# Kernel tuning notes

Hardware: AMD Instinct MI355X
Metric: run time of the kernel (lower is better)

Reference implementation:

```python
import jax, jax.numpy as jnp
from jax import lax
import numpy as np

B, L, C, PRED = 64, 512, 321, 96
PATCH, STRIDE = 16, 8
N = (L - PATCH) // STRIDE + 1 + 1  # 64 patches (after replication pad)
HID = PATCH * 2                    # expansion_factor=2
ALPHA, EPS = 0.2, 1e-5

def gelu(v):
    return jax.nn.gelu(v, approximate=False)  # torch nn.GELU default (erf)

def setup_inputs() -> dict:
    key = jax.random.key(0)
    ks = jax.random.split(key, 10)
    init = lambda k, s: (jax.random.normal(k, s) * 0.02).astype(jnp.float32)
    return dict(
        x=jax.random.normal(ks[0], (B, L, C), jnp.float32),
        rev_w=jnp.ones((C,), jnp.float32), rev_b=jnp.zeros((C,), jnp.float32),
        fc1_w=init(ks[1], (HID, PATCH)), fc1_b=jnp.zeros((HID,), jnp.float32),
        bn1_w=jnp.ones((N,), jnp.float32), bn1_b=jnp.zeros((N,), jnp.float32),
        conv_w=init(ks[2], (N, 1, 3)), conv_b=jnp.zeros((N,), jnp.float32),
        bn2_w=jnp.ones((N,), jnp.float32), bn2_b=jnp.zeros((N,), jnp.float32),
        fc2_w=init(ks[3], (PATCH, HID)), fc2_b=jnp.zeros((PATCH,), jnp.float32),
        m1_w=init(ks[4], (2 * N, N)), m1_b=jnp.zeros((2 * N,), jnp.float32),
        m2_w=init(ks[5], (N, 2 * N)), m2_b=jnp.zeros((N,), jnp.float32),
        gl_scale=jnp.full((1,), 0.1, jnp.float32),
        ln_w=jnp.ones((PATCH,), jnp.float32), ln_b=jnp.zeros((PATCH,), jnp.float32),
        seas_w=init(ks[6], (PRED, N * PATCH)), seas_b=jnp.zeros((PRED,), jnp.float32),
        tr_w=init(ks[7], (PRED, L)), tr_b=jnp.zeros((PRED,), jnp.float32),
        fus_w=init(ks[8], (PRED, 2 * PRED)), fus_b=jnp.zeros((PRED,), jnp.float32),
    )

def _batchnorm(h, w, b):
    # BatchNorm1d over channel axis N (train-mode batch stats, biased var)
    mu = h.mean((0, 2), keepdims=True)
    var = h.var((0, 2), keepdims=True)
    return (h - mu) * lax.rsqrt(var + EPS) * w[None, :, None] + b[None, :, None]

def reference(x, rev_w, rev_b, fc1_w, fc1_b, bn1_w, bn1_b, conv_w, conv_b,
              bn2_w, bn2_b, fc2_w, fc2_b, m1_w, m1_b, m2_w, m2_b, gl_scale,
              ln_w, ln_b, seas_w, seas_b, tr_w, tr_b, fus_w, fus_b):
    # --- RevIN norm (torch std is unbiased, ddof=1) ---
    mean = x.mean(1, keepdims=True)
    std = jnp.std(x, axis=1, ddof=1, keepdims=True) + EPS
    xn = (x - mean) / std * rev_w + rev_b
    # --- EMA trend/seasonal decomposition via scan ---
    xt = jnp.moveaxis(xn, 1, 0)                      # [L,B,C]
    def step(c, xi):
        t = ALPHA * xi + (1.0 - ALPHA) * c
        return t, t
    _, rest = lax.scan(step, xt[0], xt[1:])
    trend = jnp.moveaxis(jnp.concatenate([xt[:1], rest], 0), 0, 1)  # [B,L,C]
    seasonal = xn - trend
    # --- patching (replication pad right by STRIDE, unfold) ---
    s = seasonal.transpose(0, 2, 1).reshape(B * C, L)
    s = jnp.concatenate([s, jnp.broadcast_to(s[:, -1:], (B * C, STRIDE))], axis=1)
    idx = np.arange(N)[:, None] * STRIDE + np.arange(PATCH)[None, :]
    sp = s[:, idx]                                    # [B*C, N, PATCH]
    # --- IntraPatch (local): fc1 -> GELU -> BN -> depthwise conv -> GELU -> BN -> fc2 + res ---
    h = gelu(sp @ fc1_w.T + fc1_b)                    # [BC,N,HID]
    h = _batchnorm(h, bn1_w, bn1_b)
    h = lax.conv_general_dilated(h, conv_w, (1,), ((1, 1),),
                                 feature_group_count=N,
                                 dimension_numbers=('NCH', 'OIH', 'NCH'))
    h = h + conv_b[None, :, None]
    h = _batchnorm(gelu(h), bn2_w, bn2_b)
    local = h @ fc2_w.T + fc2_b + sp                  # dropout is identity (eval)
    # --- InterPatch (global): pool -> MLP -> sigmoid gate ---
    pooled = sp.mean(-1)                              # [BC,N]
    w = jax.nn.sigmoid(gelu(pooled @ m1_w.T + m1_b) @ m2_w.T + m2_b)
    glob = sp * (1.0 + gl_scale * w[..., None])
    # --- fusion 'add' + residual LayerNorm over PATCH ---
    y = sp + local + glob
    mu = y.mean(-1, keepdims=True)
    var = y.var(-1, keepdims=True)
    y = (y - mu) * lax.rsqrt(var + EPS) * ln_w + ln_b
    # --- heads ---
    s_pred = y.reshape(B * C, N * PATCH) @ seas_w.T + seas_b
    t = trend.transpose(0, 2, 1).reshape(B * C, L)
    t_pred = t @ tr_w.T + tr_b
    out = jnp.concatenate([s_pred, t_pred], -1) @ fus_w.T + fus_b
    out = out.reshape(B, C, PRED).transpose(0, 2, 1)  # [B,PRED,C]
    # --- RevIN denorm ---
    out = (out - rev_b) / rev_w
    return out * std + mean
```

## Files before the change

### kernel.cpp

```cpp
#include <hip/hip_runtime.h>
#include <hip/hip_bf16.h>
#include <hip/hip_fp16.h>
#include <math.h>

#define B_    64
#define L_    512
#define C_    321
#define PRED_ 96
#define N_    64
#define HID_  32
#define BC_   (B_*C_)
#define SROW_ 528
#define EPS_  1e-5f
#define ALPHA_ 0.2f
#define GR_   16
#define RB_   8
#define NBLK2_ (BC_/GR_)
#define NBLKH_ (BC_/8)
#define D64_  6.2771017353866808e-7f
#define STW_  548
#define UTW_  260

typedef __attribute__((ext_vector_type(8))) short bf16x8;
typedef __attribute__((ext_vector_type(4))) float f32x4;

__device__ __forceinline__ float gelu_f(float x){
  float ax = fabsf(x);
  float z  = ax * 0.70710678118654752440f;
  float t  = __builtin_amdgcn_rcpf(fmaf(0.3275911f, z, 1.0f));
  float poly = fmaf(fmaf(fmaf(fmaf(1.061405429f, t, -1.453152027f),
                   t, 1.421413741f), t, -0.284496736f), t, 0.254829592f) * t;
  float e  = __expf(-z*z);
  float erfp = fmaf(-poly, e, 1.0f);
  return fmaf(0.5f*ax, erfp, 0.5f*x);
}
__device__ __forceinline__ unsigned short bf16bits(float x){
  __hip_bfloat16 h = __float2bfloat16(x);
  return *(unsigned short*)&h;
}
__device__ __forceinline__ unsigned short f16bits(float x){
  __half h = __float2half(x);
  return *(unsigned short*)&h;
}
__device__ __forceinline__ float f16val(unsigned short u){
  __half h = *(__half*)&u;
  return __half2float(h);
}
__device__ __forceinline__ bf16x8 cvt8(const float* p){
  float4 a = *(const float4*)p;
  float4 b = *(const float4*)(p+4);
  bf16x8 v;
  v[0]=(short)bf16bits(a.x); v[1]=(short)bf16bits(a.y);
  v[2]=(short)bf16bits(a.z); v[3]=(short)bf16bits(a.w);
  v[4]=(short)bf16bits(b.x); v[5]=(short)bf16bits(b.y);
  v[6]=(short)bf16bits(b.z); v[7]=(short)bf16bits(b.w);
  return v;
}

__global__ __launch_bounds__(256) void k1_all(
    const float* __restrict__ x, const float* __restrict__ rev_w, const float* __restrict__ rev_b,
    const float* __restrict__ seas_w, const float* __restrict__ tr_w, const float* __restrict__ fus_w,
    const float* __restrict__ seas_b, const float* __restrict__ tr_b, const float* __restrict__ fus_b,
    const float* __restrict__ fc2_w,
    float* __restrict__ s_raw, __hip_bfloat16* __restrict__ t_bf, float* __restrict__ rowpar,
    float* __restrict__ pooled,
    __hip_bfloat16* __restrict__ Wsf, __hip_bfloat16* __restrict__ Wtf,
    float* __restrict__ biasc, float* __restrict__ colsumT, float* __restrict__ Wsum) {
  __shared__ float lf[8][32];
  __shared__ float psum[8][32], psq[8][32];
  __shared__ float fs[8][32];
  __shared__ float st[32*STW_];
  int tid = threadIdx.x;
  int bid = blockIdx.x;
  if (bid >= BC_/32) {
    int fb = bid - BC_/32;
    if (fb < 576) {
      int idx = fb*256 + tid;
      int j = idx / 1536, k = idx - j*1536;
      float acc = 0.f;
      if (k < 1024) {
        for (int i=0;i<96;++i) acc = fmaf(fus_w[j*192+i], seas_w[i*1024+k], acc);
        Wsf[(size_t)j*1024 + k] = __float2bfloat16(acc);
      } else {
        int l = k - 1024;
        for (int i=0;i<96;++i) acc = fmaf(fus_w[j*192+96+i], tr_w[i*512+l], acc);
        Wtf[(size_t)j*512 + l] = __float2bfloat16(acc);
      }
    } else {
      __shared__ float rowsum[96];
      if (tid >= 96 && tid < 112) {
        int j = tid - 96;
        float s = 0.f;
        #pragma unroll
        for (int k=0;k<32;++k) s += fc2_w[j*32+k];
        Wsum[j] = s;
      }
      if (tid < 96) {
        float s = 0.f;
        for (int l=0;l<512;++l) s += tr_w[tid*512+l];
        rowsum[tid] = s;
      }
      __syncthreads();
      if (tid < 96) {
        float acc = fus_b[tid], cs = 0.f;
        for (int i=0;i<96;++i) {
          acc = fmaf(fus_w[tid*192+i],    seas_b[i], acc);
          acc = fmaf(fus_w[tid*192+96+i], tr_b[i],   acc);
          cs  = fmaf(fus_w[tid*192+96+i], rowsum[i], cs);
        }
        biasc[tid] = acc; colsumT[tid] = cs;
      }
    }
    return;
  }
  int q = tid >> 5, r = tid & 31;
  int row0 = bid*32;
  int row = row0 + r;
  int b = row / C_, c = row - b*C_;
  const float* xp = x + (size_t)b*L_*C_ + c;
  int l0 = q*64;
  float sreg[64];
  float loc = 0.f, sum = 0.f, sq = 0.f;
  #pragma unroll
  for (int i=0;i<64;++i) {
    float v = xp[(size_t)(l0+i)*C_];
    sum += v; sq = fmaf(v,v,sq);
    loc = (q==0 && i==0) ? v : fmaf(ALPHA_, v, 0.8f*loc);
    sreg[i] = loc;
  }
  lf[q][r] = loc; psum[q][r] = sum; psq[q][r] = sq;
  __syncthreads();
  float cin = 0.f;
  for (int j=0;j<q;++j) cin = fmaf(D64_, cin, lf[j][r]);
  float S=0.f, Q=0.f;
  #pragma unroll
  for (int qq=0;qq<8;++qq){ S += psum[qq][r]; Q += psq[qq][r]; }
  float mean = S*(1.0f/512.0f);
  float var  = (Q - S*S*(1.0f/512.0f))*(1.0f/511.0f);
  var = fmaxf(var, 0.f);
  float stdv = sqrtf(var) + EPS_;
  float rwc = rev_w[c];
  float a = rwc / stdv;
  if (q==0) {
    float rbc = rev_b[c];
    float g = rbc - mean*a;
    float inva = stdv / rwc;
    ((float4*)rowpar)[row] = make_float4(a, g, mean, inva);
  }
  float prev = 0.f, f = 1.f, slast = 0.f;
  float sums8[8];
  #pragma unroll
  for (int j=0;j<8;++j) sums8[j] = 0.f;
  #pragma unroll
  for (int i=0;i<64;++i) {
    float lc = sreg[i];
    f *= 0.8f;
    float s = (q==0 && i==0) ? 0.f : fmaf(4.f, lc - prev, -f*cin);
    prev = lc;
    float sv = s * a;
    st[r*STW_ + q*64 + i] = sv;
    sums8[i>>3] += sv;
    slast = sv;
  }
  fs[q][r] = sums8[0];
  if (q==7) {
    #pragma unroll
    for (int k=0;k<8;++k) st[r*STW_ + 512 + k] = slast;
  }
  __syncthreads();
  for (int idx=tid; idx<32*130; idx+=256) {
    int rr = idx/130, g = idx - rr*130;
    float4 v = *(float4*)&st[rr*STW_ + g*4];
    *(float4*)&s_raw[(size_t)(row0+rr)*SROW_ + g*4] = v;
  }
  {
    float nf = (q < 7) ? fs[q+1][r] : 8.0f*slast;
    #pragma unroll
    for (int j=0;j<7;++j)
      pooled[(size_t)row*64 + q*8 + j] = (sums8[j] + sums8[j+1])*(1.0f/16.0f);
    pooled[(size_t)row*64 + q*8 + 7] = (sums8[7] + nf)*(1.0f/16.0f);
  }
  __syncthreads();
  unsigned* tb = (unsigned*)st;
  {
    float f2 = 1.f; unsigned lo = 0;
    #pragma unroll
    for (int i=0;i<64;++i) {
      f2 *= 0.8f;
      float tt = fmaf(f2, cin, sreg[i]) * a;
      unsigned hb = bf16bits(tt);
      if ((i&1)==0) lo = hb;
      else tb[r*UTW_ + q*32 + (i>>1)] = lo | (hb<<16);
    }
  }
  __syncthreads();
  for (int idx=tid; idx<32*64; idx+=256) {
    int rr = idx>>6, g = idx&63;
    uint4 v = *(uint4*)&tb[rr*UTW_ + g*4];
    *(uint4*)&t_bf[(size_t)(row0+rr)*512 + g*8] = v;
  }
}

__global__ __launch_bounds__(512) void k4_gate(
    const float* __restrict__ pooled,
    const float* __restrict__ m1_w, const float* __restrict__ m1_b,
    const float* __restrict__ m2_w, const float* __restrict__ m2_b,
    float* __restrict__ wl_g) {
  __shared__ __align__(16) __hip_bfloat16 buf[17408];
  int t = threadIdx.x;
  int row0 = blockIdx.x*64;
  __hip_bfloat16* A1 = buf;
  __hip_bfloat16* B1 = buf + 4608;
  __hip_bfloat16* H1 = buf;
  __hip_bfloat16* B2 = buf + 8704;
  for (int idx=t; idx<4096; idx+=512) {
    int r = idx>>6, k = idx&63;
    A1[r*72+k] = __float2bfloat16(pooled[(size_t)(row0+r)*64 + k]);
  }
  for (int idx=t; idx<8192; idx+=512) {
    int r = idx>>6, k = idx&63;
    B1[r*72+k] = __float2bfloat16(m1_w[idx]);
  }
  __syncthreads();
  int lane = t & 63, w = t >> 6;
  int fr = lane & 15, fg = lane >> 4;
  int mt = w & 3;
  int ng0 = (w>>2)*4;
  f32x4 acc1[4];
  #pragma unroll
  for (int nn=0;nn<4;++nn) acc1[nn] = (f32x4){0.f,0.f,0.f,0.f};
  #pragma unroll
  for (int ksub=0; ksub<2; ++ksub) {
    bf16x8 av = *(bf16x8*)&A1[(mt*16+fr)*72 + ksub*32 + fg*8];
    #pragma unroll
    for (int nn=0;nn<4;++nn) {
      bf16x8 bv = *(bf16x8*)&B1[((ng0+nn)*16+fr)*72 + ksub*32 + fg*8];
      acc1[nn] = __builtin_amdgcn_mfma_f32_16x16x32_bf16(av, bv, acc1[nn], 0,0,0);
    }
  }
  __syncthreads();
  #pragma unroll
  for (int nn=0;nn<4;++nn) {
    int col = (ng0+nn)*16 + fr;
    float bias = m1_b[col];
    #pragma unroll
    for (int reg=0;reg<4;++reg) {
      int row = mt*16 + fg*4 + reg;
      H1[row*136 + col] = __float2bfloat16(gelu_f(acc1[nn][reg] + bias));
    }
  }
  for (int idx=t; idx<8192; idx+=512) {
    int r = idx>>7, k = idx&127;
    B2[r*136+k] = __float2bfloat16(m2_w[idx]);
  }
  __syncthreads();
  int nt0 = (w>>2)*2;
  f32x4 acc2[2];
  #pragma unroll
  for (int nn=0;nn<2;++nn) acc2[nn] = (f32x4){0.f,0.f,0.f,0.f};
  #pragma unroll
  for (int ksub=0; ksub<4; ++ksub) {
    bf16x8 av = *(bf16x8*)&H1[(mt*16+fr)*136 + ksub*32 + fg*8];
    #pragma unroll
    for (int nn=0;nn<2;++nn) {
      bf16x8 bv = *(bf16x8*)&B2[((nt0+nn)*16+fr)*136 + ksub*32 + fg*8];
      acc2[nn] = __builtin_amdgcn_mfma_f32_16x16x32_bf16(av, bv, acc2[nn], 0,0,0);
    }
  }
  #pragma unroll
  for (int nn=0;nn<2;++nn) {
    int col = (nt0+nn)*16 + fr;
    float bias = m2_b[col];
    #pragma unroll
    for (int reg=0;reg<4;++reg) {
      int row = mt*16 + fg*4 + reg;
      wl_g[(size_t)(row0+row)*64 + col] = 1.0f/(1.0f + __expf(-(acc2[nn][reg] + bias)));
    }
  }
}

__global__ __launch_bounds__(256) void k2_bn1stats(
    const float* __restrict__ s_raw,
    const float* __restrict__ fc1_w, const float* __restrict__ fc1_b,
    float* __restrict__ partials) {
  __shared__ float sl[GR_*SROW_];
  __shared__ float red[2][GR_*64];
  int t = threadIdx.x;
  int row0 = blockIdx.x*GR_;
  for (int idx=t; idx<GR_*520; idx+=256) {
    int rr = idx/520, cc = idx - rr*520;
    sl[rr*SROW_+cc] = s_raw[(size_t)(row0+rr)*SROW_+cc];
  }
  __syncthreads();
  int lr = t >> 4, ng = t & 15;
  for (int q=0;q<4;++q) {
    int n = ng + 16*q;
    float sp[16];
    #pragma unroll
    for (int p=0;p<16;++p) sp[p] = sl[lr*SROW_ + n*8 + p];
    float s1=0.f, s2=0.f;
    #pragma unroll
    for (int hid=0; hid<32; ++hid) {
      float acc = fc1_b[hid];
      #pragma unroll
      for (int p=0;p<16;++p) acc = fmaf(sp[p], fc1_w[hid*16+p], acc);
      float gv = gelu_f(acc);
      s1 += gv; s2 = fmaf(gv,gv,s2);
    }
    red[0][lr*64+n] = s1;
    red[1][lr*64+n] = s2;
  }
  __syncthreads();
  if (t < 64) {
    float S1=0.f, S2=0.f;
    for (int lr2=0; lr2<GR_; ++lr2) { S1 += red[0][lr2*64+t]; S2 += red[1][lr2*64+t]; }
    partials[((size_t)blockIdx.x*64+t)*2+0] = S1;
    partials[((size_t)blockIdx.x*64+t)*2+1] = S2;
  }
}

__global__ __launch_bounds__(512) void k2v5_bn1_cr(
    const float* __restrict__ s_raw,
    const float* __restrict__ fc1_w, const float* __restrict__ fc1_b,
    const float* __restrict__ conv_w,
    float* __restrict__ partials, __hip_bfloat16* __restrict__ crp) {
  __shared__ __align__(16) __hip_bfloat16 Hb[4*512*8];
  __shared__ float cw[192];
  __shared__ float red[2][512];
  int t = threadIdx.x;
  int row0 = blockIdx.x*8;
  if (t < 192) cw[t] = conv_w[t];
  int lane = t & 63, w = t >> 6;
  int fr = lane & 15, fg = lane >> 4;
  bf16x8 z8 = (bf16x8){0,0,0,0,0,0,0,0};
  bf16x8 wv0 = (fg < 2) ? cvt8(&fc1_w[(0*16+fr)*16 + fg*8]) : z8;
  bf16x8 wv1 = (fg < 2) ? cvt8(&fc1_w[(1*16+fr)*16 + fg*8]) : z8;
  f32x4 acc[4][2];
  #pragma unroll
  for (int mt=0;mt<4;++mt)
    #pragma unroll
    for (int nt=0;nt<2;++nt) acc[mt][nt] = (f32x4){0.f,0.f,0.f,0.f};
  #pragma unroll
  for (int mt=0;mt<4;++mt) {
    int p = (w*4+mt)*16 + fr;
    int lr = p>>6, n = p&63;
    bf16x8 pv = (fg < 2) ? cvt8(&s_raw[(size_t)(row0+lr)*SROW_ + n*8 + fg*8]) : z8;
    acc[mt][0] = __builtin_amdgcn_mfma_f32_16x16x32_bf16(wv0, pv, acc[mt][0], 0,0,0);
    acc[mt][1] = __builtin_amdgcn_mfma_f32_16x16x32_bf16(wv1, pv, acc[mt][1], 0,0,0);
  }
  #pragma unroll
  for (int mt=0;mt<4;++mt) {
    int p = (w*4+mt)*16 + fr;
    #pragma unroll
    for (int nt=0;nt<2;++nt) {
      float4 b4 = ((const float4*)fc1_b)[nt*4+fg];
      float g0 = gelu_f(acc[mt][nt][0] + b4.x);
      float g1 = gelu_f(acc[mt][nt][1] + b4.y);
      float g2 = gelu_f(acc[mt][nt][2] + b4.z);
      float g3 = gelu_f(acc[mt][nt][3] + b4.w);
      unsigned lo = (unsigned)bf16bits(g0) | (((unsigned)bf16bits(g1))<<16);
      unsigned hi = (unsigned)bf16bits(g2) | (((unsigned)bf16bits(g3))<<16);
      int hb = nt*16 + fg*4;
      *(uint2*)&Hb[(hb>>3)*4096 + p*8 + (hb&7)] = make_uint2(lo, hi);
    }
  }
  __syncthreads();
  {
    int n = t & 63;
    uint4 u0 = *(const uint4*)&Hb[0*4096 + t*8];
    uint4 u1 = *(const uint4*)&Hb[1*4096 + t*8];
    uint4 u2 = *(const uint4*)&Hb[2*4096 + t*8];
    uint4 u3 = *(const uint4*)&Hb[3*4096 + t*8];
    unsigned uw[16] = {u0.x,u0.y,u0.z,u0.w, u1.x,u1.y,u1.z,u1.w,
                       u2.x,u2.y,u2.z,u2.w, u3.x,u3.y,u3.z,u3.w};
    float g[32];
    #pragma unroll
    for (int j=0;j<16;++j) {
      g[2*j]   = __uint_as_float(uw[j]<<16);
      g[2*j+1] = __uint_as_float(uw[j] & 0xffff0000u);
    }
    float s1=0.f, s2=0.f;
    #pragma unroll
    for (int k=0;k<32;++k) { s1 += g[k]; s2 = fmaf(g[k], g[k], s2); }
    float w0=cw[n*3], wm=cw[n*3+1], wp=cw[n*3+2];
    unsigned wds[16]; unsigned crlo = 0;
    float prevv = 0.f;
    #pragma unroll
    for (int k=0;k<32;++k) {
      float cr = fmaf(prevv, w0, fmaf(g[k], wm, (k<31) ? g[k+1]*wp : 0.f));
      prevv = g[k];
      unsigned hbits = bf16bits(cr);
      if ((k&1)==0) crlo = hbits; else wds[k>>1] = crlo | (hbits<<16);
    }
    uint4* dst = (uint4*)&crp[((size_t)row0*64 + t)*32];
    dst[0] = make_uint4(wds[0],wds[1],wds[2],wds[3]);
    dst[1] = make_uint4(wds[4],wds[5],wds[6],wds[7]);
    dst[2] = make_uint4(wds[8],wds[9],wds[10],wds[11]);
    dst[3] = make_uint4(wds[12],wds[13],wds[14],wds[15]);
    red[0][t] = s1;
    red[1][t] = s2;
  }
  __syncthreads();
  if (t < 64) {
    float S1=0.f, S2=0.f;
    #pragma unroll
    for (int lr2=0; lr2<8; ++lr2) { S1 += red[0][lr2*64+t]; S2 += red[1][lr2*64+t]; }
    partials[((size_t)blockIdx.x*64+t)*2+0] = S1;
    partials[((size_t)blockIdx.x*64+t)*2+1] = S2;
  }
}

__global__ __launch_bounds__(256) void k_bnreduce(
    const float* __restrict__ partials, int nblk,
    const float* __restrict__ bnw, const float* __restrict__ bnb,
    float* __restrict__ scale, float* __restrict__ shift) {
  __shared__ float red[2][256];
  int n = blockIdx.x, t = threadIdx.x;
  float s1=0.f, s2=0.f;
  for (int i=t; i<nblk; i+=256) {
    s1 += partials[((size_t)i*64+n)*2+0];
    s2 += partials[((size_t)i*64+n)*2+1];
  }
  red[0][t]=s1; red[1][t]=s2;
  __syncthreads();
  for (int off=128; off>0; off>>=1) {
    if (t<off) { red[0][t]+=red[0][t+off]; red[1][t]+=red[1][t+off]; }
    __syncthreads();
  }
  if (t==0) {
    const float count = (float)BC_ * 32.0f;
    float mu = red[0][0]/count;
    float var = red[1][0]/count - mu*mu;
    float sc = rsqrtf(var + EPS_) * bnw[n];
    scale[n] = sc;
    shift[n] = bnb[n] - mu*sc;
  }
}

__global__ __launch_bounds__(256) void k3_bn2stats(
    const float* __restrict__ s_raw,
    const float* __restrict__ fc1_w, const float* __restrict__ fc1_b,
    const float* __restrict__ scale1, const float* __restrict__ shift1,
    const float* __restrict__ conv_w, const float* __restrict__ conv_b,
    float* __restrict__ partials) {
  __shared__ float sl[GR_*SROW_];
  __shared__ float sc1[64], sh1[64], cw[192], cb[64];
  __shared__ float red[2][GR_*64];
  int t = threadIdx.x;
  int row0 = blockIdx.x*GR_;
  if (t < 64) { sc1[t]=scale1[t]; sh1[t]=shift1[t]; cb[t]=conv_b[t]; }
  if (t >= 64 && t < 256) cw[t-64] = conv_w[t-64];
  __syncthreads();
  for (int idx=t; idx<GR_*520; idx+=256) {
    int rr = idx/520, cc = idx - rr*520;
    sl[rr*SROW_+cc] = s_raw[(size_t)(row0+rr)*SROW_+cc];
  }
  __syncthreads();
  int lr = t >> 4, ng = t & 15;
  for (int q=0;q<4;++q) {
    int n = ng + 16*q;
    float sp[16];
    #pragma unroll
    for (int p=0;p<16;++p) sp[p] = sl[lr*SROW_ + n*8 + p];
    float scn = sc1[n], shn = sh1[n];
    float h[32];
    #pragma unroll
    for (int hid=0; hid<32; ++hid) {
      float acc = fc1_b[hid];
      #pragma unroll
      for (int p=0;p<16;++p) acc = fmaf(sp[p], fc1_w[hid*16+p], acc);
      h[hid] = fmaf(gelu_f(acc), scn, shn);
    }
    float w0=cw[n*3], wm=cw[n*3+1], wpp=cw[n*3+2], cbn=cb[n];
    float s1=0.f, s2=0.f, prev=0.f;
    #pragma unroll
    for (int k2=0;k2<32;++k2) {
      float cur = h[k2];
      float cv = cbn;
      cv = fmaf(prev, w0, cv);
      cv = fmaf(cur, wm, cv);
      if (k2<31) cv = fmaf(h[k2+1], wpp, cv);
      float gv = gelu_f(cv);
      s1 += gv; s2 = fmaf(gv,gv,s2);
      prev = cur;
    }
    red[0][lr*64+n]=s1; red[1][lr*64+n]=s2;
  }
  __syncthreads();
  if (t < 64) {
    float S1=0.f, S2=0.f;
    for (int lr2=0; lr2<GR_; ++lr2) { S1 += red[0][lr2*64+t]; S2 += red[1][lr2*64+t]; }
    partials[((size_t)blockIdx.x*64+t)*2+0] = S1;
    partials[((size_t)blockIdx.x*64+t)*2+1] = S2;
  }
}

__global__ __launch_bounds__(512) void k3v3_bn2_u(
    const __hip_bfloat16* __restrict__ crp,
    const float* __restrict__ scale1, const float* __restrict__ shift1,
    const float* __restrict__ conv_w, const float* __restrict__ conv_b,
    const float* __restrict__ fc2_w,
    float* __restrict__ partials, __half* __restrict__ Ub) {
  __shared__ float sc1[64], sh0l[64], shml[64], sh31l[64];
  __shared__ float red[2][512];
  int t = threadIdx.x;
  int row0 = blockIdx.x*8;
  if (t < 64) {
    float w0=conv_w[t*3], wm=conv_w[t*3+1], wp=conv_w[t*3+2];
    float s1v=shift1[t], cbv=conv_b[t];
    sc1[t]  = scale1[t];
    sh0l[t] = fmaf(s1v, wm+wp, cbv);
    shml[t] = fmaf(s1v, w0+wm+wp, cbv);
    sh31l[t]= fmaf(s1v, w0+wm, cbv);
  }
  __syncthreads();
  int n = t&63;
  const uint4* crb = (const uint4*)&crp[((size_t)row0*64 + t)*32];
  uint4 u0=crb[0], u1=crb[1], u2=crb[2], u3=crb[3];
  unsigned uw[16] = {u0.x,u0.y,u0.z,u0.w, u1.x,u1.y,u1.z,u1.w,
                     u2.x,u2.y,u2.z,u2.w, u3.x,u3.y,u3.z,u3.w};
  float sc1n = sc1[n];
  float shm = shml[n];
  float g[32];
  float s1=0.f, s2=0.f;
  #pragma unroll
  for (int j=0;j<16;++j) {
    unsigned u = uw[j];
    float c0 = __uint_as_float(u<<16);
    float c1 = __uint_as_float(u & 0xffff0000u);
    float sh_0 = (j==0)  ? sh0l[n]  : shm;
    float sh_1 = (j==15) ? sh31l[n] : shm;
    float g0 = gelu_f(fmaf(c0, sc1n, sh_0));
    float g1 = gelu_f(fmaf(c1, sc1n, sh_1));
    g[2*j]   = g0;
    g[2*j+1] = g1;
    s1 += g0 + g1;
    s2 = fmaf(g0,g0, fmaf(g1,g1, s2));
  }
  unsigned wds[8];
  #pragma unroll
  for (int jj=0;jj<8;++jj) {
    float ua = 0.f, ub = 0.f;
    #pragma unroll
    for (int k=0;k<32;++k) {
      ua = fmaf(fc2_w[(2*jj  )*32+k], g[k], ua);
      ub = fmaf(fc2_w[(2*jj+1)*32+k], g[k], ub);
    }
    wds[jj] = (unsigned)f16bits(ua) | (((unsigned)f16bits(ub))<<16);
  }
  uint4* dst = (uint4*)&Ub[((size_t)row0*64 + t)*16];
  dst[0] = make_uint4(wds[0],wds[1],wds[2],wds[3]);
  dst[1] = make_uint4(wds[4],wds[5],wds[6],wds[7]);
  red[0][t]=s1; red[1][t]=s2;
  __syncthreads();
  if (t < 64) {
    float S1=0.f, S2=0.f;
    #pragma unroll
    for (int lr2=0; lr2<8; ++lr2) { S1 += red[0][lr2*64+t]; S2 += red[1][lr2*64+t]; }
    partials[((size_t)blockIdx.x*64+t)*2+0] = S1;
    partials[((size_t)blockIdx.x*64+t)*2+1] = S2;
  }
}

__global__ __launch_bounds__(256) void k5a_pipeline(
    const float* __restrict__ s_raw, const float* __restrict__ wl_g,
    const float* __restrict__ fc1_w, const float* __restrict__ fc1_b,
    const float* __restrict__ scale1, const float* __restrict__ shift1,
    const float* __restrict__ conv_w, const float* __restrict__ conv_b,
    const float* __restrict__ scale2, const float* __restrict__ shift2,
    const float* __restrict__ fc2_w, const float* __restrict__ fc2_b,
    const float* __restrict__ gl_scale,
    const float* __restrict__ ln_w, const float* __restrict__ ln_b,
    __hip_bfloat16* __restrict__ ybf) {
  __shared__ float sl[RB_*SROW_];
  __shared__ float cw[192], cb[64];
  __shared__ float sc1[64], sh1[64], sc2[64], sh2[64];
  int t = threadIdx.x;
  int row0 = blockIdx.x*RB_;
  if (t<64) { sc1[t]=scale1[t]; sh1[t]=shift1[t]; sc2[t]=scale2[t]; sh2[t]=shift2[t]; cb[t]=conv_b[t]; }
  if (t>=64 && t<256) cw[t-64]=conv_w[t-64];
  __syncthreads();
  for (int idx=t; idx<RB_*520; idx+=256) {
    int rr = idx/520, cc = idx - rr*520;
    sl[rr*SROW_+cc] = s_raw[(size_t)(row0+rr)*SROW_+cc];
  }
  __syncthreads();
  float glv = gl_scale[0];
  for (int idx=t; idx<RB_*64; idx+=256) {
    int rr = idx>>6, n = idx&63;
    float wlv = wl_g[(size_t)row0*64 + idx];
    float h[32];
    {
      float sp[16];
      #pragma unroll
      for (int p=0;p<16;++p) sp[p] = sl[rr*SROW_ + n*8 + p];
      float scn=sc1[n], shn=sh1[n];
      #pragma unroll
      for (int hid=0;hid<32;++hid) {
        float acc=fc1_b[hid];
        #pragma unroll
        for (int p=0;p<16;++p) acc=fmaf(sp[p], fc1_w[hid*16+p], acc);
        h[hid]=fmaf(gelu_f(acc), scn, shn);
      }
    }
    {
      float w0=cw[n*3], wm=cw[n*3+1], wpp=cw[n*3+2], cbn=cb[n];
      float sc2n=sc2[n], sh2n=sh2[n];
      float prev=0.f;
      #pragma unroll
      for (int k2=0;k2<32;++k2) {
        float cur = h[k2];
        float cv = cbn;
        cv = fmaf(prev, w0, cv);
        cv = fmaf(cur, wm, cv);
        if (k2<31) cv = fmaf(h[k2+1], wpp, cv);
        h[k2] = fmaf(gelu_f(cv), sc2n, sh2n);
        prev = cur;
      }
    }
    float yv[16];
    #pragma unroll
    for (int p=0;p<16;++p) {
      float acc=fc2_b[p];
      #pragma unroll
      for (int hid=0;hid<32;++hid) acc=fmaf(h[hid], fc2_w[p*32+hid], acc);
      yv[p]=acc;
    }
    float smul = 3.0f + glv*wlv;
    float mu=0.f;
    #pragma unroll
    for (int p=0;p<16;++p) {
      yv[p]=fmaf(sl[rr*SROW_ + n*8 + p], smul, yv[p]);
      mu+=yv[p];
    }
    mu *= (1.0f/16.0f);
    float var=0.f;
    #pragma unroll
    for (int p=0;p<16;++p){ float d=yv[p]-mu; var=fmaf(d,d,var); }
    var *= (1.0f/16.0f);
    float rs = rsqrtf(var + EPS_);
    unsigned int wds[8];
    #pragma unroll
    for (int j=0;j<8;++j) {
      unsigned int lo = bf16bits(fmaf((yv[2*j]-mu)*rs,   ln_w[2*j],   ln_b[2*j]));
      unsigned int hi = bf16bits(fmaf((yv[2*j+1]-mu)*rs, ln_w[2*j+1], ln_b[2*j+1]));
      wds[j] = lo | (hi<<16);
    }
    size_t ybase = (size_t)(row0+rr)*1024 + n*16;
    uint4* dst = (uint4*)&ybf[ybase];
    dst[0] = make_uint4(wds[0],wds[1],wds[2],wds[3]);
    dst[1] = make_uint4(wds[4],wds[5],wds[6],wds[7]);
  }
}

__global__ __launch_bounds__(512) void k5a_v4(
    const float* __restrict__ s_raw, const float* __restrict__ wl_g,
    const float* __restrict__ scale2, const float* __restrict__ shift2,
    const float* __restrict__ Wsum, const float* __restrict__ fc2_b,
    const float* __restrict__ gl_scale,
    const float* __restrict__ ln_w, const float* __restrict__ ln_b,
    __hip_bfloat16* __restrict__ ybf) {
  __shared__ float sc2l[64], sh2l[64];
  int t = threadIdx.x;
  int row0 = blockIdx.x*RB_;
  if (t < 64) { sc2l[t]=scale2[t]; sh2l[t]=shift2[t]; }
  __syncthreads();
  int rr = t>>6, n = t&63;
  int row = row0 + rr;
  float glv = gl_scale[0];
  float wlv = wl_g[(size_t)row*64 + n];
  size_t pbase = ((size_t)row*64 + n)*16;
  uint4* uptr = (uint4*)&ybf[pbase];
  uint4 a = uptr[0], b = uptr[1];
  unsigned hw[8] = {a.x,a.y,a.z,a.w, b.x,b.y,b.z,b.w};
  float sc2n = sc2l[n], sh2n = sh2l[n];
  float yv[16];
  #pragma unroll
  for (int j=0;j<8;++j) {
    float U0 = f16val((unsigned short)(hw[j] & 0xffffu));
    float U1 = f16val((unsigned short)(hw[j] >> 16));
    yv[2*j]   = fmaf(sc2n, U0, fmaf(sh2n, Wsum[2*j],   fc2_b[2*j]));
    yv[2*j+1] = fmaf(sc2n, U1, fmaf(sh2n, Wsum[2*j+1], fc2_b[2*j+1]));
  }
  const float* sp_g = &s_raw[(size_t)row*SROW_ + n*8];
  float4 s0 = *(const float4*)(sp_g);
  float4 s1v = *(const float4*)(sp_g+4);
  float4 s2v = *(const float4*)(sp_g+8);
  float4 s3 = *(const float4*)(sp_g+12);
  float sp[16] = {s0.x,s0.y,s0.z,s0.w, s1v.x,s1v.y,s1v.z,s1v.w,
                  s2v.x,s2v.y,s2v.z,s2v.w, s3.x,s3.y,s3.z,s3.w};
  float smul = 3.0f + glv*wlv;
  float mu=0.f;
  #pragma unroll
  for (int p=0;p<16;++p) {
    yv[p] = fmaf(sp[p], smul, yv[p]);
    mu += yv[p];
  }
  mu *= (1.0f/16.0f);
  float var=0.f;
  #pragma unroll
  for (int p=0;p<16;++p){ float d=yv[p]-mu; var=fmaf(d,d,var); }
  var *= (1.0f/16.0f);
  float rs = rsqrtf(var + EPS_);
  unsigned int wds[8];
  #pragma unroll
  for (int j=0;j<8;++j) {
    unsigned int lo = bf16bits(fmaf((yv[2*j]-mu)*rs,   ln_w[2*j],   ln_b[2*j]));
    unsigned int hi = bf16bits(fmaf((yv[2*j+1]-mu)*rs, ln_w[2*j+1], ln_b[2*j+1]));
    wds[j] = lo | (hi<<16);
  }
  uptr[0] = make_uint4(wds[0],wds[1],wds[2],wds[3]);
  uptr[1] = make_uint4(wds[4],wds[5],wds[6],wds[7]);
}

__global__ __launch_bounds__(384) void k5b_gemm(
    const __hip_bfloat16* __restrict__ ybf, const __hip_bfloat16* __restrict__ tbf,
    const __hip_bfloat16* __restrict__ Wsf, const __hip_bfloat16* __restrict__ Wtf,
    const float* __restrict__ rowpar, const float* __restrict__ rev_b,
    const float* __restrict__ biasc, const float* __restrict__ colsumT,
    float* __restrict__ out) {
  __shared__ __align__(16) __hip_bfloat16 As[2*16*72];
  __shared__ __align__(16) __hip_bfloat16 Bs[2*96*72];
  __shared__ float rp[64];
  __shared__ float rbl[16];
  __shared__ int   obase[16];
  __shared__ float bcl[96], csl[96];
  int tid = threadIdx.x;
  int row0 = blockIdx.x*16;
  if (tid < 64) rp[tid] = rowpar[(size_t)row0*4 + tid];
  if (tid >= 64 && tid < 80) {
    int lr = tid-64;
    int row = row0 + lr; int b = row/C_; int c = row - b*C_;
    rbl[lr] = rev_b[c]; obase[lr] = b*PRED_*C_ + c;
  }
  if (tid >= 96 && tid < 192) { bcl[tid-96]=biasc[tid-96]; csl[tid-96]=colsumT[tid-96]; }
  int lane = tid & 63, w = tid >> 6;
  int fr = lane & 15, fg = lane >> 4;
  bool a0 = tid < 128;
  int r0 = a0 ? (tid>>3) : ((tid-128)>>3);
  int c0 = a0 ? (tid&7)  : ((tid-128)&7);
  int r1 = (tid+256)>>3, c1 = (tid+256)&7;
  bool h2 = tid < 128;
  int r2 = (tid+640)>>3, c2 = (tid+640)&7;
  f32x4 acc = (f32x4){0.f,0.f,0.f,0.f};

  uint4 v0, v1, v2;
  auto LOAD = [&](int ks){
    const __hip_bfloat16* Ag; const __hip_bfloat16* Bg; int K; int kofs;
    if (ks < 8) { Ag = tbf + (size_t)row0*512;  Bg = Wtf; K = 512;  kofs = ks*64; }
    else        { Ag = ybf + (size_t)row0*1024; Bg = Wsf; K = 1024; kofs = (ks-8)*64; }
    v0 = a0 ? *(const uint4*)(Ag + (size_t)r0*K + kofs + c0*8)
            : *(const uint4*)(Bg + (size_t)r0*K + kofs + c0*8);
    v1 = *(const uint4*)(Bg + (size_t)r1*K + kofs + c1*8);
    if (h2) v2 = *(const uint4*)(Bg + (size_t)r2*K + kofs + c2*8);
  };

  LOAD(0);
  int cur = 0;
  for (int ks=0; ks<24; ++ks) {
    __hip_bfloat16* Ab = &As[cur*16*72];
    __hip_bfloat16* Bb = &Bs[cur*96*72];
    if (a0) *(uint4*)&Ab[r0*72 + c0*8] = v0;
    else    *(uint4*)&Bb[r0*72 + c0*8] = v0;
    *(uint4*)&Bb[r1*72 + c1*8] = v1;
    if (h2) *(uint4*)&Bb[r2*72 + c2*8] = v2;
    __syncthreads();
    if (ks < 23) LOAD(ks+1);
    #pragma unroll
    for (int ksub=0; ksub<2; ++ksub) {
      bf16x8 av = *(bf16x8*)&Ab[fr*72 + ksub*32 + fg*8];
      bf16x8 bv = *(bf16x8*)&Bb[(w*16+fr)*72 + ksub*32 + fg*8];
      acc = __builtin_amdgcn_mfma_f32_16x16x32_bf16(av, bv, acc, 0,0,0);
    }
    cur ^= 1;
  }
  {
    int col = w*16 + fr;
    float cs = csl[col], bc = bcl[col];
    #pragma unroll
    for (int reg=0;reg<4;++reg) {
      int rloc = fg*4 + reg;
      float g = rp[rloc*4+1], meanv = rp[rloc*4+2], inva = rp[rloc*4+3];
      float val = acc[reg] + g*cs + bc;
      val = (val - rbl[rloc])*inva + meanv;
      out[(size_t)obase[rloc] + (size_t)col*C_] = val;
    }
  }
}

extern "C" void kernel_launch(void* const* d_in, const int* in_sizes, int n_in,
                              void* d_out, int out_size, void* d_ws, size_t ws_size,
                              hipStream_t stream) {
  const float* x      = (const float*)d_in[0];
  const float* rev_w  = (const float*)d_in[1];
  const float* rev_b  = (const float*)d_in[2];
  const float* fc1_w  = (const float*)d_in[3];
  const float* fc1_b  = (const float*)d_in[4];
  const float* bn1_w  = (const float*)d_in[5];
  const float* bn1_b  = (const float*)d_in[6];
  const float* conv_w = (const float*)d_in[7];
  const float* conv_b = (const float*)d_in[8];
  const float* bn2_w  = (const float*)d_in[9];
  const float* bn2_b  = (const float*)d_in[10];
  const float* fc2_w  = (const float*)d_in[11];
  const float* fc2_b  = (const float*)d_in[12];
  const float* m1_w   = (const float*)d_in[13];
  const float* m1_b   = (const float*)d_in[14];
  const float* m2_w   = (const float*)d_in[15];
  const float* m2_b   = (const float*)d_in[16];
  const float* gl     = (const float*)d_in[17];
  const float* ln_w   = (const float*)d_in[18];
  const float* ln_b   = (const float*)d_in[19];
  const float* seas_w = (const float*)d_in[20];
  const float* seas_b = (const float*)d_in[21];
  const float* tr_w   = (const float*)d_in[22];
  const float* tr_b   = (const float*)d_in[23];
  const float* fus_w  = (const float*)d_in[24];
  const float* fus_b  = (const float*)d_in[25];
  float* out = (float*)d_out;
  float* ws = (float*)d_ws;

  __hip_bfloat16* Wsf  = (__hip_bfloat16*)(ws);
  __hip_bfloat16* Wtf  = (__hip_bfloat16*)(ws + 49152);
  float* biasc   = ws + 73728;
  float* colsumT = ws + 73856;
  float* scale1  = ws + 73984;
  float* shift1  = ws + 74048;
  float* scale2  = ws + 74112;
  float* shift2  = ws + 74176;
  float* partials= ws + 74240;
  float* Wsum    = ws + 74240;
  float* rowpar  = ws + 238592;
  float* s_raw   = ws + 320768;
  __hip_bfloat16* t_bf = (__hip_bfloat16*)(ws + 11168000);
  __hip_bfloat16* ybf  = (__hip_bfloat16*)(ws + 16427264);
  float* pooled  = ws + 26945792;
  float* wl_g    = ws + 28260608;
  __hip_bfloat16* crp  = (__hip_bfloat16*)(ws + 29575424);
  float* ppool   = ws + 26945792;
  __half* Uh     = (__half*)ybf;
  const size_t NEED = (29575424ull + 21037056ull) * 4ull;
  bool big = (ws_size >= NEED);

  hipLaunchKernelGGL(k1_all, dim3(BC_/32 + 577), dim3(256), 0, stream,
    x, rev_w, rev_b, seas_w, tr_w, fus_w, seas_b, tr_b, fus_b, fc2_w,
    s_raw, t_bf, rowpar, pooled, Wsf, Wtf, biasc, colsumT, Wsum);
  hipLaunchKernelGGL(k4_gate, dim3(BC_/64), dim3(512), 0, stream, pooled, m1_w, m1_b, m2_w, m2_b, wl_g);
  if (big) {
    hipLaunchKernelGGL(k2v5_bn1_cr, dim3(NBLKH_), dim3(512), 0, stream, s_raw, fc1_w, fc1_b, conv_w, ppool, crp);
    hipLaunchKernelGGL(k_bnreduce, dim3(64), dim3(256), 0, stream, ppool, NBLKH_, bn1_w, bn1_b, scale1, shift1);
    hipLaunchKernelGGL(k3v3_bn2_u, dim3(NBLKH_), dim3(512), 0, stream, crp, scale1, shift1, conv_w, conv_b, fc2_w, ppool, Uh);
    hipLaunchKernelGGL(k_bnreduce, dim3(64), dim3(256), 0, stream, ppool, NBLKH_, bn2_w, bn2_b, scale2, shift2);
    hipLaunchKernelGGL(k5a_v4, dim3(NBLKH_), dim3(512), 0, stream,
      s_raw, wl_g, scale2, shift2, Wsum, fc2_b, gl, ln_w, ln_b, ybf);
  } else {
    hipLaunchKernelGGL(k2_bn1stats, dim3(NBLK2_), dim3(256), 0, stream, s_raw, fc1_w, fc1_b, partials);
    hipLaunchKernelGGL(k_bnreduce, dim3(64), dim3(256), 0, stream, partials, NBLK2_, bn1_w, bn1_b, scale1, shift1);
    hipLaunchKernelGGL(k3_bn2stats, dim3(NBLK2_), dim3(256), 0, stream, s_raw, fc1_w, fc1_b, scale1, shift1, conv_w, conv_b, partials);
    hipLaunchKernelGGL(k_bnreduce, dim3(64), dim3(256), 0, stream, partials, NBLK2_, bn2_w, bn2_b, scale2, shift2);
    hipLaunchKernelGGL(k5a_pipeline, dim3(BC_/RB_), dim3(256), 0, stream,
      s_raw, wl_g, fc1_w, fc1_b, scale1, shift1, conv_w, conv_b,
      scale2, shift2, fc2_w, fc2_b, gl, ln_w, ln_b, ybf);
  }
  hipLaunchKernelGGL(k5b_gemm, dim3(BC_/16), dim3(384), 0, stream,
    ybf, t_bf, Wsf, Wtf, rowpar, rev_b, biasc, colsumT, out);
}
```

Baseline: 206.9 us.

## Recompute fc1+GELU+conv in BN2 kernel instead of storing intermediate conv tensor

The BN1 stats kernel no longer writes the bf16 conv-result intermediate (crp). It only computes the fc1 MFMA, applies GELU and reduces sums directly from registers. The BN2 kernel now rereads s_raw and recomputes fc1, GELU and the depthwise conv before applying BN1, GELU and fc2. This trades a large intermediate global write and read for duplicated MFMA and GELU compute plus an extra s_raw read, and adds register pressure from the fused loop.

```diff
diff --git a/kernel.cpp b/kernel.cpp
--- a/kernel.cpp
+++ b/kernel.cpp
@@ -319,92 +319,48 @@
   }
 }
 
-__global__ __launch_bounds__(512) void k2v5_bn1_cr(
+__global__ __launch_bounds__(512) void k2v6_bn1stats(
     const float* __restrict__ s_raw,
     const float* __restrict__ fc1_w, const float* __restrict__ fc1_b,
-    const float* __restrict__ conv_w,
-    float* __restrict__ partials, __hip_bfloat16* __restrict__ crp) {
-  __shared__ __align__(16) __hip_bfloat16 Hb[4*512*8];
-  __shared__ float cw[192];
-  __shared__ float red[2][512];
+    float* __restrict__ partials) {
+  __shared__ float red[2][4][16][33];
   int t = threadIdx.x;
   int row0 = blockIdx.x*8;
-  if (t < 192) cw[t] = conv_w[t];
   int lane = t & 63, w = t >> 6;
   int fr = lane & 15, fg = lane >> 4;
   bf16x8 z8 = (bf16x8){0,0,0,0,0,0,0,0};
-  bf16x8 wv0 = (fg < 2) ? cvt8(&fc1_w[(0*16+fr)*16 + fg*8]) : z8;
-  bf16x8 wv1 = (fg < 2) ? cvt8(&fc1_w[(1*16+fr)*16 + fg*8]) : z8;
-  f32x4 acc[4][2];
-  #pragma unroll
-  for (int mt=0;mt<4;++mt)
-    #pragma unroll
-    for (int nt=0;nt<2;++nt) acc[mt][nt] = (f32x4){0.f,0.f,0.f,0.f};
+  bf16x8 wv0 = (fg < 2) ? cvt8(&fc1_w[fr*16 + fg*8]) : z8;
+  bf16x8 wv1 = (fg < 2) ? cvt8(&fc1_w[(16+fr)*16 + fg*8]) : z8;
+  float4 b40 = ((const float4*)fc1_b)[fg];
+  float4 b41 = ((const float4*)fc1_b)[4+fg];
   #pragma unroll
   for (int mt=0;mt<4;++mt) {
     int p = (w*4+mt)*16 + fr;
     int lr = p>>6, n = p&63;
     bf16x8 pv = (fg < 2) ? cvt8(&s_raw[(size_t)(row0+lr)*SROW_ + n*8 + fg*8]) : z8;
-    acc[mt][0] = __builtin_amdgcn_mfma_f32_16x16x32_bf16(wv0, pv, acc[mt][0], 0,0,0);
-    acc[mt][1] = __builtin_amdgcn_mfma_f32_16x16x32_bf16(wv1, pv, acc[mt][1], 0,0,0);
-  }
-  #pragma unroll
-  for (int mt=0;mt<4;++mt) {
-    int p = (w*4+mt)*16 + fr;
-    #pragma unroll
-    for (int nt=0;nt<2;++nt) {
-      float4 b4 = ((const float4*)fc1_b)[nt*4+fg];
-      float g0 = gelu_f(acc[mt][nt][0] + b4.x);
-      float g1 = gelu_f(acc[mt][nt][1] + b4.y);
-      float g2 = gelu_f(acc[mt][nt][2] + b4.z);
-      float g3 = gelu_f(acc[mt][nt][3] + b4.w);
-      unsigned lo = (unsigned)bf16bits(g0) | (((unsigned)bf16bits(g1))<<16);
-      unsigned hi = (unsigned)bf16bits(g2) | (((unsigned)bf16bits(g3))<<16);
-      int hb = nt*16 + fg*4;
-      *(uint2*)&Hb[(hb>>3)*4096 + p*8 + (hb&7)] = make_uint2(lo, hi);
-    }
-  }
-  __syncthreads();
-  {
-    int n = t & 63;
-    uint4 u0 = *(const uint4*)&Hb[0*4096 + t*8];
-    uint4 u1 = *(const uint4*)&Hb[1*4096 + t*8];
-    uint4 u2 = *(const uint4*)&Hb[2*4096 + t*8];
-    uint4 u3 = *(const uint4*)&Hb[3*4096 + t*8];
-    unsigned uw[16] = {u0.x,u0.y,u0.z,u0.w, u1.x,u1.y,u1.z,u1.w,
-                       u2.x,u2.y,u2.z,u2.w, u3.x,u3.y,u3.z,u3.w};
-    float g[32];
-    #pragma unroll
-    for (int j=0;j<16;++j) {
-      g[2*j]   = __uint_as_float(uw[j]<<16);
-      g[2*j+1] = __uint_as_float(uw[j] & 0xffff0000u);
-    }
+    f32x4 a0 = (f32x4){0.f,0.f,0.f,0.f};
+    f32x4 a1 = (f32x4){0.f,0.f,0.f,0.f};
+    a0 = __builtin_amdgcn_mfma_f32_16x16x32_bf16(wv0, pv, a0, 0,0,0);
+    a1 = __builtin_amdgcn_mfma_f32_16x16x32_bf16(wv1, pv, a1, 0,0,0);
     float s1=0.f, s2=0.f;
-    #pragma unroll
-    for (int k=0;k<32;++k) { s1 += g[k]; s2 = fmaf(g[k], g[k], s2); }
-    float w0=cw[n*3], wm=cw[n*3+1], wp=cw[n*3+2];
-    unsigned wds[16]; unsigned crlo = 0;
-    float prevv = 0.f;
-    #pragma unroll
-    for (int k=0;k<32;++k) {
-      float cr = fmaf(prevv, w0, fmaf(g[k], wm, (k<31) ? g[k+1]*wp : 0.f));
-      prevv = g[k];
-      unsigned hbits = bf16bits(cr);
-      if ((k&1)==0) crlo = hbits; else wds[k>>1] = crlo | (hbits<<16);
-    }
-    uint4* dst = (uint4*)&crp[((size_t)row0*64 + t)*32];
-    dst[0] = make_uint4(wds[0],wds[1],wds[2],wds[3]);
-    dst[1] = make_uint4(wds[4],wds[5],wds[6],wds[7]);
-    dst[2] = make_uint4(wds[8],wds[9],wds[10],wds[11]);
-    dst[3] = make_uint4(wds[12],wds[13],wds[14],wds[15]);
-    red[0][t] = s1;
-    red[1][t] = s2;
+    float bb0[4] = {b40.x,b40.y,b40.z,b40.w};
+    float bb1[4] = {b41.x,b41.y,b41.z,b41.w};
+    #pragma unroll
+    for (int reg=0;reg<4;++reg) {
+      float g0 = gelu_f(a0[reg] + bb0[reg]);
+      float g1 = gelu_f(a1[reg] + bb1[reg]);
+      s1 += g0 + g1;
+      s2 = fmaf(g0,g0, fmaf(g1,g1, s2));
+    }
+    red[0][mt][fr][w*4+fg] = s1;
+    red[1][mt][fr][w*4+fg] = s2;
   }
   __syncthreads();
   if (t < 64) {
+    int mtn = t>>4, frn = t&15;
     float S1=0.f, S2=0.f;
     #pragma unroll
-    for (int lr2=0; lr2<8; ++lr2) { S1 += red[0][lr2*64+t]; S2 += red[1][lr2*64+t]; }
+    for (int i=0;i<32;++i) { S1 += red[0][mtn][frn][i]; S2 += red[1][mtn][frn][i]; }
     partials[((size_t)blockIdx.x*64+t)*2+0] = S1;
     partials[((size_t)blockIdx.x*64+t)*2+1] = S2;
   }
@@ -495,13 +451,16 @@
   }
 }
 
-__global__ __launch_bounds__(512) void k3v3_bn2_u(
-    const __hip_bfloat16* __restrict__ crp,
+__global__ __launch_bounds__(512) void k3v4_bn2_u(
+    const float* __restrict__ s_raw,
+    const float* __restrict__ fc1_w, const float* __restrict__ fc1_b,
     const float* __restrict__ scale1, const float* __restrict__ shift1,
     const float* __restrict__ conv_w, const float* __restrict__ conv_b,
     const float* __restrict__ fc2_w,
     float* __restrict__ partials, __half* __restrict__ Ub) {
+  __shared__ __align__(16) __hip_bfloat16 Hb[4*512*8];
   __shared__ float sc1[64], sh0l[64], shml[64], sh31l[64];
+  __shared__ float cw[192];
   __shared__ float red[2][512];
   int t = threadIdx.x;
   int row0 = blockIdx.x*8;
@@ -513,45 +472,82 @@
     shml[t] = fmaf(s1v, w0+wm+wp, cbv);
     sh31l[t]= fmaf(s1v, w0+wm, cbv);
   }
-  __syncthreads();
-  int n = t&63;
-  const uint4* crb = (const uint4*)&crp[((size_t)row0*64 + t)*32];
-  uint4 u0=crb[0], u1=crb[1], u2=crb[2], u3=crb[3];
-  unsigned uw[16] = {u0.x,u0.y,u0.z,u0.w, u1.x,u1.y,u1.z,u1.w,
-                     u2.x,u2.y,u2.z,u2.w, u3.x,u3.y,u3.z,u3.w};
-  float sc1n = sc1[n];
-  float shm = shml[n];
-  float g[32];
-  float s1=0.f, s2=0.f;
-  #pragma unroll
-  for (int j=0;j<16;++j) {
-    unsigned u = uw[j];
-    float c0 = __uint_as_float(u<<16);
-    float c1 = __uint_as_float(u & 0xffff0000u);
-    float sh_0 = (j==0)  ? sh0l[n]  : shm;
-    float sh_1 = (j==15) ? sh31l[n] : shm;
-    float g0 = gelu_f(fmaf(c0, sc1n, sh_0));
-    float g1 = gelu_f(fmaf(c1, sc1n, sh_1));
-    g[2*j]   = g0;
-    g[2*j+1] = g1;
-    s1 += g0 + g1;
-    s2 = fmaf(g0,g0, fmaf(g1,g1, s2));
-  }
-  unsigned wds[8];
-  #pragma unroll
-  for (int jj=0;jj<8;++jj) {
-    float ua = 0.f, ub = 0.f;
+  if (t >= 64 && t < 256) cw[t-64] = conv_w[t-64];
+  int lane = t & 63, w = t >> 6;
+  int fr = lane & 15, fg = lane >> 4;
+  bf16x8 z8 = (bf16x8){0,0,0,0,0,0,0,0};
+  bf16x8 wv0 = (fg < 2) ? cvt8(&fc1_w[fr*16 + fg*8]) : z8;
+  bf16x8 wv1 = (fg < 2) ? cvt8(&fc1_w[(16+fr)*16 + fg*8]) : z8;
+  f32x4 acc[4][2];
+  #pragma unroll
+  for (int mt=0;mt<4;++mt)
+    #pragma unroll
+    for (int nt=0;nt<2;++nt) acc[mt][nt] = (f32x4){0.f,0.f,0.f,0.f};
+  #pragma unroll
+  for (int mt=0;mt<4;++mt) {
+    int p = (w*4+mt)*16 + fr;
+    int lr = p>>6, n = p&63;
+    bf16x8 pv = (fg < 2) ? cvt8(&s_raw[(size_t)(row0+lr)*SROW_ + n*8 + fg*8]) : z8;
+    acc[mt][0] = __builtin_amdgcn_mfma_f32_16x16x32_bf16(wv0, pv, acc[mt][0], 0,0,0);
+    acc[mt][1] = __builtin_amdgcn_mfma_f32_16x16x32_bf16(wv1, pv, acc[mt][1], 0,0,0);
+  }
+  #pragma unroll
+  for (int mt=0;mt<4;++mt) {
+    int p = (w*4+mt)*16 + fr;
+    #pragma unroll
+    for (int nt=0;nt<2;++nt) {
+      float4 b4 = ((const float4*)fc1_b)[nt*4+fg];
+      float g0 = gelu_f(acc[mt][nt][0] + b4.x);
+      float g1 = gelu_f(acc[mt][nt][1] + b4.y);
+      float g2 = gelu_f(acc[mt][nt][2] + b4.z);
+      float g3 = gelu_f(acc[mt][nt][3] + b4.w);
+      unsigned lo = (unsigned)bf16bits(g0) | (((unsigned)bf16bits(g1))<<16);
+      unsigned hi = (unsigned)bf16bits(g2) | (((unsigned)bf16bits(g3))<<16);
+      int hb = nt*16 + fg*4;
+      *(uint2*)&Hb[(hb>>3)*4096 + p*8 + (hb&7)] = make_uint2(lo, hi);
+    }
+  }
+  __syncthreads();
+  {
+    int n = t & 63;
+    uint4 u0 = *(const uint4*)&Hb[0*4096 + t*8];
+    uint4 u1 = *(const uint4*)&Hb[1*4096 + t*8];
+    uint4 u2 = *(const uint4*)&Hb[2*4096 + t*8];
+    uint4 u3 = *(const uint4*)&Hb[3*4096 + t*8];
+    unsigned uw[16] = {u0.x,u0.y,u0.z,u0.w, u1.x,u1.y,u1.z,u1.w,
+                       u2.x,u2.y,u2.z,u2.w, u3.x,u3.y,u3.z,u3.w};
+    float g[32];
+    #pragma unroll
+    for (int j=0;j<16;++j) {
+      g[2*j]   = __uint_as_float(uw[j]<<16);
+      g[2*j+1] = __uint_as_float(uw[j] & 0xffff0000u);
+    }
+    float w0=cw[n*3], wm=cw[n*3+1], wp=cw[n*3+2];
+    float sc1n = sc1[n];
+    float shm = shml[n], sh0 = sh0l[n], sh31 = sh31l[n];
+    float u[16];
+    #pragma unroll
+    for (int jj=0;jj<16;++jj) u[jj] = 0.f;
+    float s1=0.f, s2=0.f, prevv=0.f;
     #pragma unroll
     for (int k=0;k<32;++k) {
-      ua = fmaf(fc2_w[(2*jj  )*32+k], g[k], ua);
-      ub = fmaf(fc2_w[(2*jj+1)*32+k], g[k], ub);
-    }
-    wds[jj] = (unsigned)f16bits(ua) | (((unsigned)f16bits(ub))<<16);
-  }
-  uint4* dst = (uint4*)&Ub[((size_t)row0*64 + t)*16];
-  dst[0] = make_uint4(wds[0],wds[1],wds[2],wds[3]);
-  dst[1] = make_uint4(wds[4],wds[5],wds[6],wds[7]);
-  red[0][t]=s1; red[1][t]=s2;
+      float cr = fmaf(prevv, w0, fmaf(g[k], wm, (k<31) ? g[k+1]*wp : 0.f));
+      prevv = g[k];
+      float sh = (k==0) ? sh0 : ((k==31) ? sh31 : shm);
+      float gv = gelu_f(fmaf(cr, sc1n, sh));
+      s1 += gv; s2 = fmaf(gv,gv,s2);
+      #pragma unroll
+      for (int jj=0;jj<16;++jj) u[jj] = fmaf(fc2_w[jj*32+k], gv, u[jj]);
+    }
+    unsigned wds[8];
+    #pragma unroll
+    for (int jj=0;jj<8;++jj)
+      wds[jj] = (unsigned)f16bits(u[2*jj]) | (((unsigned)f16bits(u[2*jj+1]))<<16);
+    uint4* dst = (uint4*)&Ub[((size_t)row0*64 + t)*16];
+    dst[0] = make_uint4(wds[0],wds[1],wds[2],wds[3]);
+    dst[1] = make_uint4(wds[4],wds[5],wds[6],wds[7]);
+    red[0][t]=s1; red[1][t]=s2;
+  }
   __syncthreads();
   if (t < 64) {
     float S1=0.f, S2=0.f;
@@ -836,7 +832,6 @@
   __hip_bfloat16* ybf  = (__hip_bfloat16*)(ws + 16427264);
   float* pooled  = ws + 26945792;
   float* wl_g    = ws + 28260608;
-  __hip_bfloat16* crp  = (__hip_bfloat16*)(ws + 29575424);
   float* ppool   = ws + 26945792;
   __half* Uh     = (__half*)ybf;
   const size_t NEED = (29575424ull + 21037056ull) * 4ull;
@@ -847,9 +842,10 @@
     s_raw, t_bf, rowpar, pooled, Wsf, Wtf, biasc, colsumT, Wsum);
   hipLaunchKernelGGL(k4_gate, dim3(BC_/64), dim3(512), 0, stream, pooled, m1_w, m1_b, m2_w, m2_b, wl_g);
   if (big) {
-    hipLaunchKernelGGL(k2v5_bn1_cr, dim3(NBLKH_), dim3(512), 0, stream, s_raw, fc1_w, fc1_b, conv_w, ppool, crp);
+    hipLaunchKernelGGL(k2v6_bn1stats, dim3(NBLKH_), dim3(512), 0, stream, s_raw, fc1_w, fc1_b, ppool);
     hipLaunchKernelGGL(k_bnreduce, dim3(64), dim3(256), 0, stream, ppool, NBLKH_, bn1_w, bn1_b, scale1, shift1);
-    hipLaunchKernelGGL(k3v3_bn2_u, dim3(NBLKH_), dim3(512), 0, stream, crp, scale1, shift1, conv_w, conv_b, fc2_w, ppool, Uh);
+    hipLaunchKernelGGL(k3v4_bn2_u, dim3(NBLKH_), dim3(512), 0, stream,
+      s_raw, fc1_w, fc1_b, scale1, shift1, conv_w, conv_b, fc2_w, ppool, Uh);
     hipLaunchKernelGGL(k_bnreduce, dim3(64), dim3(256), 0, stream, ppool, NBLKH_, bn2_w, bn2_b, scale2, shift2);
     hipLaunchKernelGGL(k5a_v4, dim3(NBLKH_), dim3(512), 0, stream,
       s_raw, wl_g, scale2, shift2, Wsum, fc2_b, gl, ln_w, ln_b, ybf);
```

Result: slower. 226.1 us (+9.3%).
